# Optimization experiments

Measured on AMD Instinct MI355X. Metric: run time of the kernel, lower is better.

The kernel has to match this reference:

```python
import jax, jax.numpy as jnp
import numpy as np

SIZE = (8, 8, 256, 256)          # target [X_out, Y_out, U_out, V_out]
ALIGN_CORNERS = True
IN_SHAPE = (1, 16, 5, 5, 128, 128)  # [N, C, X, Y, U, V]


def _lerp_axis(x, out_size, axis, align_corners=True):
    """1D linear interpolation along `axis` (multilinear interp is separable,
    so applying this along X,Y,U,V is exactly quadrilinear / 16-corner interp)."""
    in_size = x.shape[axis]
    if align_corners:
        scale = (in_size - 1) / (out_size - 1) if out_size > 1 else 0.0
        coords = jnp.arange(out_size, dtype=jnp.float32) * scale
    else:
        scale = in_size / out_size
        coords = (jnp.arange(out_size, dtype=jnp.float32) + 0.5) * scale - 0.5
        coords = jnp.clip(coords, 0.0, float(in_size - 1))
    i0 = jnp.clip(jnp.floor(coords).astype(jnp.int32), 0, in_size - 1)
    i1 = jnp.minimum(i0 + 1, in_size - 1)
    w = coords - i0.astype(jnp.float32)
    # broadcast weight along `axis`
    wshape = [1] * x.ndim
    wshape[axis] = out_size
    w = w.reshape(wshape).astype(x.dtype)
    x0 = jnp.take(x, i0, axis=axis)
    x1 = jnp.take(x, i1, axis=axis)
    return x0 + (x1 - x0) * w


def setup_inputs() -> dict:
    key = jax.random.key(0)
    inp = jax.random.normal(key, IN_SHAPE, dtype=jnp.float32)
    return {"input": inp}


@jax.jit
def reference(input) -> jnp.ndarray:
    # input: [N, C, X, Y, U, V] -> [N, C, *SIZE]
    out = input
    for d, out_size in enumerate(SIZE):
        out = _lerp_axis(out, out_size, axis=2 + d, align_corners=ALIGN_CORNERS)
    return out
```

## Files before the change

### kernel.cpp

```cpp
#include <hip/hip_runtime.h>


constexpr int C  = 16;
constexpr int IX = 5,  IY = 5,  IU = 128, IV = 128;
constexpr int OX = 8,  OY = 8,  OU = 256, OV = 256;
constexpr int QROWS = 64;
constexpr int SROWS = 34;

typedef float floatx4 __attribute__((ext_vector_type(4)));

__global__ __launch_bounds__(256) void interp4d(const float* __restrict__ in,
                                                float* __restrict__ out) {
    __shared__ float plane[SROWS * IV];

    const int b  = blockIdx.x;
    const int q  = b & 3;
    const int yo = (b >> 2) & 7;
    const int xo = (b >> 5) & 7;
    const int c  = b >> 8;

    const float sxy = (float)(4.0 / 7.0);
    float cx = (float)xo * sxy;
    int   x0 = (int)cx;            x0 = x0 > IX - 1 ? IX - 1 : x0;
    int   x1 = x0 + 1 < IX ? x0 + 1 : IX - 1;
    float wx = cx - (float)x0;

    float cy = (float)yo * sxy;
    int   y0 = (int)cy;            y0 = y0 > IY - 1 ? IY - 1 : y0;
    int   y1 = y0 + 1 < IY ? y0 + 1 : IY - 1;
    float wy = cy - (float)y0;

    const float w00 = (1.f - wx) * (1.f - wy);
    const float w01 = (1.f - wx) * wy;
    const float w10 = wx * (1.f - wy);
    const float w11 = wx * wy;

    const float suv = (float)(127.0 / 255.0);

    const int ubase = (int)((float)(q * QROWS) * suv);

    const size_t planeSz = (size_t)IU * IV;
    const floatx4* p00 = (const floatx4*)(in + ((size_t)(c * IX + x0) * IY + y0) * planeSz);
    const floatx4* p01 = (const floatx4*)(in + ((size_t)(c * IX + x0) * IY + y1) * planeSz);
    const floatx4* p10 = (const floatx4*)(in + ((size_t)(c * IX + x1) * IY + y0) * planeSz);
    const floatx4* p11 = (const floatx4*)(in + ((size_t)(c * IX + x1) * IY + y1) * planeSz);

    floatx4* lp = (floatx4*)plane;
    for (int i = threadIdx.x; i < SROWS * (IV / 4); i += 256) {
        int r  = i >> 5;
        int cl = i & 31;
        int gr = ubase + r;  gr = gr > IU - 1 ? IU - 1 : gr;
        int gi = gr * (IV / 4) + cl;
        floatx4 a  = p00[gi];
        floatx4 b2 = p01[gi];
        floatx4 c2 = p10[gi];
        floatx4 d2 = p11[gi];
        lp[i] = w00 * a + w01 * b2 + w10 * c2 + w11 * d2;
    }
    __syncthreads();

    const int lane = threadIdx.x & 63;
    const int wg   = threadIdx.x >> 6;

    int   vi0[4], vi1[4];
    float vw[4];
#pragma unroll
    for (int j = 0; j < 4; ++j) {
        int   vo = lane * 4 + j;
        float cv = (float)vo * suv;
        int   v0 = (int)cv;        v0 = v0 > IV - 1 ? IV - 1 : v0;
        vi0[j] = v0;
        vi1[j] = v0 + 1 < IV ? v0 + 1 : IV - 1;
        vw[j]  = cv - (float)v0;
    }

    float* obase = out + (((size_t)(c * OX + xo) * OY + yo) * OU + q * QROWS) * OV;

    for (int ul = wg; ul < QROWS; ul += 4) {
        int   uo = q * QROWS + ul;
        float cu = (float)uo * suv;
        int   u0 = (int)cu;        u0 = u0 > IU - 1 ? IU - 1 : u0;
        int   u1 = u0 + 1 < IU ? u0 + 1 : IU - 1;
        float wu = cu - (float)u0;

        const float* r0 = plane + (u0 - ubase) * IV;
        const float* r1 = plane + (u1 - ubase) * IV;

        float tmp[4];
#pragma unroll
        for (int j = 0; j < 4; ++j) {
            float a  = r0[vi0[j]];
            float bb = r0[vi1[j]];
            float cc = r1[vi0[j]];
            float dd = r1[vi1[j]];
            float t0 = a  + (cc - a ) * wu;
            float t1 = bb + (dd - bb) * wu;
            tmp[j]   = t0 + (t1 - t0) * vw[j];
        }
        floatx4 res;
        res.x = tmp[0]; res.y = tmp[1]; res.z = tmp[2]; res.w = tmp[3];
        __builtin_nontemporal_store(res, (floatx4*)(obase + (size_t)ul * OV) + lane);
    }
}

extern "C" void kernel_launch(void* const* d_in, const int* in_sizes, int n_in,
                              void* d_out, int out_size, void* d_ws, size_t ws_size,
                              hipStream_t stream) {
    const float* in  = (const float*)d_in[0];
    float*       out = (float*)d_out;
    interp4d<<<dim3(C * OX * OY * 4), dim3(256), 0, stream>>>(in, out);
}
```

Before: 58.23 us.

## Process 2x2 output XY tiles per block to reuse input plane loads

Each block now produces four (xo,yo) output planes that share the same pair of input X/Y indices. It loads the four corner input planes once, writes four XY-blended planes to LDS, then interpolates along U/V for each. The V-direction gather is also replaced by four contiguous LDS reads plus selects. This cuts redundant global input reads by 4x and quarters the grid, at the cost of 4x LDS per block (about 70KB), which lowers occupancy and leaves only 256 blocks.

```diff
diff --git a/kernel.cpp b/kernel.cpp
--- a/kernel.cpp
+++ b/kernel.cpp
@@ -6,100 +6,133 @@
 constexpr int OX = 8,  OY = 8,  OU = 256, OV = 256;
 constexpr int QROWS = 64;
 constexpr int SROWS = 34;
+constexpr int PLANE = SROWS * IV;
 
 typedef float floatx4 __attribute__((ext_vector_type(4)));
 
 __global__ __launch_bounds__(256) void interp4d(const float* __restrict__ in,
                                                 float* __restrict__ out) {
-    __shared__ float plane[SROWS * IV];
+    __shared__ float lds[4 * PLANE + 4];
 
     const int b  = blockIdx.x;
     const int q  = b & 3;
-    const int yo = (b >> 2) & 7;
-    const int xo = (b >> 5) & 7;
-    const int c  = b >> 8;
+    const int yp = (b >> 2) & 3;
+    const int xp = (b >> 4) & 3;
+    const int c  = b >> 6;
 
-    const float sxy = (float)(4.0 / 7.0);
-    float cx = (float)xo * sxy;
-    int   x0 = (int)cx;            x0 = x0 > IX - 1 ? IX - 1 : x0;
-    int   x1 = x0 + 1 < IX ? x0 + 1 : IX - 1;
-    float wx = cx - (float)x0;
+    const float sxy = 4.0f / 7.0f;
+    const float suv = 127.0f / 255.0f;
 
-    float cy = (float)yo * sxy;
-    int   y0 = (int)cy;            y0 = y0 > IY - 1 ? IY - 1 : y0;
-    int   y1 = y0 + 1 < IY ? y0 + 1 : IY - 1;
-    float wy = cy - (float)y0;
+    float ax[2]; int xp0;
+    {
+        float cx = (float)(2 * xp) * sxy;
+        int x0 = (int)cx; x0 = x0 > IX - 1 ? IX - 1 : x0;
+        xp0 = x0; ax[0] = cx - (float)x0;
+        cx = (float)(2 * xp + 1) * sxy;
+        x0 = (int)cx; x0 = x0 > IX - 1 ? IX - 1 : x0;
+        ax[1] = (x0 > xp0) ? 1.0f : (cx - (float)x0);
+    }
+    const int xp1 = xp0 + 1 < IX ? xp0 + 1 : IX - 1;
 
-    const float w00 = (1.f - wx) * (1.f - wy);
-    const float w01 = (1.f - wx) * wy;
-    const float w10 = wx * (1.f - wy);
-    const float w11 = wx * wy;
-
-    const float suv = (float)(127.0 / 255.0);
+    float ay[2]; int yp0;
+    {
+        float cy = (float)(2 * yp) * sxy;
+        int y0 = (int)cy; y0 = y0 > IY - 1 ? IY - 1 : y0;
+        yp0 = y0; ay[0] = cy - (float)y0;
+        cy = (float)(2 * yp + 1) * sxy;
+        y0 = (int)cy; y0 = y0 > IY - 1 ? IY - 1 : y0;
+        ay[1] = (y0 > yp0) ? 1.0f : (cy - (float)y0);
+    }
+    const int yp1 = yp0 + 1 < IY ? yp0 + 1 : IY - 1;
 
     const int ubase = (int)((float)(q * QROWS) * suv);
 
-    const size_t planeSz = (size_t)IU * IV;
-    const floatx4* p00 = (const floatx4*)(in + ((size_t)(c * IX + x0) * IY + y0) * planeSz);
-    const floatx4* p01 = (const floatx4*)(in + ((size_t)(c * IX + x0) * IY + y1) * planeSz);
-    const floatx4* p10 = (const floatx4*)(in + ((size_t)(c * IX + x1) * IY + y0) * planeSz);
-    const floatx4* p11 = (const floatx4*)(in + ((size_t)(c * IX + x1) * IY + y1) * planeSz);
+    const size_t psz = (size_t)IU * IV;
+    const floatx4* p00 = (const floatx4*)(in + ((size_t)(c * IX + xp0) * IY + yp0) * psz);
+    const floatx4* p01 = (const floatx4*)(in + ((size_t)(c * IX + xp0) * IY + yp1) * psz);
+    const floatx4* p10 = (const floatx4*)(in + ((size_t)(c * IX + xp1) * IY + yp0) * psz);
+    const floatx4* p11 = (const floatx4*)(in + ((size_t)(c * IX + xp1) * IY + yp1) * psz);
 
-    floatx4* lp = (floatx4*)plane;
+    if (threadIdx.x < 4) lds[4 * PLANE + threadIdx.x] = 0.0f;
+
+    floatx4* lp = (floatx4*)lds;
     for (int i = threadIdx.x; i < SROWS * (IV / 4); i += 256) {
         int r  = i >> 5;
-        int cl = i & 31;
-        int gr = ubase + r;  gr = gr > IU - 1 ? IU - 1 : gr;
-        int gi = gr * (IV / 4) + cl;
-        floatx4 a  = p00[gi];
-        floatx4 b2 = p01[gi];
-        floatx4 c2 = p10[gi];
-        floatx4 d2 = p11[gi];
-        lp[i] = w00 * a + w01 * b2 + w10 * c2 + w11 * d2;
+        int gr = ubase + r; gr = gr > IU - 1 ? IU - 1 : gr;
+        int gi = gr * (IV / 4) + (i & 31);
+        floatx4 a00 = p00[gi], a01 = p01[gi], a10 = p10[gi], a11 = p11[gi];
+#pragma unroll
+        for (int dy = 0; dy < 2; ++dy) {
+            floatx4 q0 = a00 + (a01 - a00) * ay[dy];
+            floatx4 q1 = a10 + (a11 - a10) * ay[dy];
+#pragma unroll
+            for (int dx = 0; dx < 2; ++dx) {
+                lp[(dx * 2 + dy) * (PLANE / 4) + i] = q0 + (q1 - q0) * ax[dx];
+            }
+        }
     }
     __syncthreads();
 
     const int lane = threadIdx.x & 63;
     const int wg   = threadIdx.x >> 6;
 
-    int   vi0[4], vi1[4];
-    float vw[4];
+    int a_; float vw0, vw1, vw2, vw3; int s1, s2, s3;
+    {
+        float cv = (float)(4 * lane) * suv;
+        int v0 = (int)cv; v0 = v0 > IV - 1 ? IV - 1 : v0;
+        a_ = v0; vw0 = cv - (float)v0;
+        cv = (float)(4 * lane + 1) * suv;
+        v0 = (int)cv; v0 = v0 > IV - 1 ? IV - 1 : v0;
+        s1 = v0 - a_; vw1 = cv - (float)v0;
+        cv = (float)(4 * lane + 2) * suv;
+        v0 = (int)cv; v0 = v0 > IV - 1 ? IV - 1 : v0;
+        s2 = v0 - a_; vw2 = cv - (float)v0;
+        cv = (float)(4 * lane + 3) * suv;
+        v0 = (int)cv; v0 = v0 > IV - 1 ? IV - 1 : v0;
+        s3 = v0 - a_; vw3 = cv - (float)v0;
+    }
+    const bool c1a = (s1 == 0), c1b = (s1 == 1);
+    const bool c2a = (s2 == 0), c2b = (s2 == 1);
+    const bool c3a = (s3 == 0), c3b = (s3 == 1);
+
+    float* ob[4];
 #pragma unroll
-    for (int j = 0; j < 4; ++j) {
-        int   vo = lane * 4 + j;
-        float cv = (float)vo * suv;
-        int   v0 = (int)cv;        v0 = v0 > IV - 1 ? IV - 1 : v0;
-        vi0[j] = v0;
-        vi1[j] = v0 + 1 < IV ? v0 + 1 : IV - 1;
-        vw[j]  = cv - (float)v0;
+    for (int m = 0; m < 4; ++m) {
+        int xo = 2 * xp + (m >> 1), yo = 2 * yp + (m & 1);
+        ob[m] = out + (((size_t)(c * OX + xo) * OY + yo) * OU + q * QROWS) * OV;
     }
-
-    float* obase = out + (((size_t)(c * OX + xo) * OY + yo) * OU + q * QROWS) * OV;
 
     for (int ul = wg; ul < QROWS; ul += 4) {
         int   uo = q * QROWS + ul;
         float cu = (float)uo * suv;
-        int   u0 = (int)cu;        u0 = u0 > IU - 1 ? IU - 1 : u0;
+        int   u0 = (int)cu; u0 = u0 > IU - 1 ? IU - 1 : u0;
         int   u1 = u0 + 1 < IU ? u0 + 1 : IU - 1;
         float wu = cu - (float)u0;
-
-        const float* r0 = plane + (u0 - ubase) * IV;
-        const float* r1 = plane + (u1 - ubase) * IV;
-
-        float tmp[4];
+        const int lr0 = (u0 - ubase) * IV + a_;
+        const int lr1 = (u1 - ubase) * IV + a_;
 #pragma unroll
-        for (int j = 0; j < 4; ++j) {
-            float a  = r0[vi0[j]];
-            float bb = r0[vi1[j]];
-            float cc = r1[vi0[j]];
-            float dd = r1[vi1[j]];
-            float t0 = a  + (cc - a ) * wu;
-            float t1 = bb + (dd - bb) * wu;
-            tmp[j]   = t0 + (t1 - t0) * vw[j];
+        for (int m = 0; m < 4; ++m) {
+            const float* r0 = lds + m * PLANE + lr0;
+            const float* r1 = lds + m * PLANE + lr1;
+            float f0 = r0[0], f1 = r0[1], f2 = r0[2], f3 = r0[3];
+            float h0 = r1[0], h1 = r1[1], h2 = r1[2], h3 = r1[3];
+            float g0 = f0 + (h0 - f0) * wu;
+            float g1 = f1 + (h1 - f1) * wu;
+            float g2 = f2 + (h2 - f2) * wu;
+            float g3 = f3 + (h3 - f3) * wu;
+            float x01 = c1a ? g0 : (c1b ? g1 : g2);
+            float x11 = c1a ? g1 : (c1b ? g2 : g3);
+            float x02 = c2a ? g0 : (c2b ? g1 : g2);
+            float x12 = c2a ? g1 : (c2b ? g2 : g3);
+            float x03 = c3a ? g0 : (c3b ? g1 : g2);
+            float x13 = c3a ? g1 : (c3b ? g2 : g3);
+            floatx4 res;
+            res.x = g0  + (g1  - g0 ) * vw0;
+            res.y = x01 + (x11 - x01) * vw1;
+            res.z = x02 + (x12 - x02) * vw2;
+            res.w = x03 + (x13 - x03) * vw3;
+            __builtin_nontemporal_store(res, (floatx4*)(ob[m] + (size_t)ul * OV) + lane);
         }
-        floatx4 res;
-        res.x = tmp[0]; res.y = tmp[1]; res.z = tmp[2]; res.w = tmp[3];
-        __builtin_nontemporal_store(res, (floatx4*)(obase + (size_t)ul * OV) + lane);
     }
 }
 
@@ -108,5 +141,5 @@
                               hipStream_t stream) {
     const float* in  = (const float*)d_in[0];
     float*       out = (float*)d_out;
-    interp4d<<<dim3(C * OX * OY * 4), dim3(256), 0, stream>>>(in, out);
+    interp4d<<<dim3(C * 4 * 4 * 4), dim3(256), 0, stream>>>(in, out);
 }
```

Result: no change. 57.66 us (-1.0%).
